# Optimization experiments

Measured on AMD Instinct MI355X. Metric: run time of the kernel, lower is better.

Reference implementation:

```python
import jax, jax.numpy as jnp
import numpy as np

N = 40000      # nodes
E = 640000     # edges (avg degree 16)
D_IN = 256     # input_size
H = 128        # hidden_size
C = 64         # num_classes
L = 2          # num_middle_layers


def spmm(val, row, col, mat):
    # sparse [N,N] @ dense [N,D]: gather neighbor rows, scale, scatter-add
    return jax.ops.segment_sum(val[:, None] * mat[col], row, num_segments=mat.shape[0])


def setup_inputs() -> dict:
    key = jax.random.key(0)
    ks = jax.random.split(key, 12)
    x = jax.random.normal(ks[0], (N, D_IN), dtype=jnp.float32)
    edge_row = jax.random.randint(ks[1], (E,), 0, N)
    edge_col = jax.random.randint(ks[2], (E,), 0, N)
    edge_val = jax.random.uniform(ks[3], (E,), dtype=jnp.float32) / 16.0  # ~normalized adjacency
    # Linear params (stored [in, out]; math equivalent to torch x @ W.T + b)
    w1 = jax.random.normal(ks[4], (D_IN, H), dtype=jnp.float32) * (1.0 / np.sqrt(D_IN))
    b1 = jax.random.normal(ks[5], (H,), dtype=jnp.float32) * 0.01
    wm = jax.random.normal(ks[6], (L, H, H), dtype=jnp.float32) * (1.0 / np.sqrt(H))
    bm = jax.random.normal(ks[7], (L, H), dtype=jnp.float32) * 0.01
    w2 = jax.random.normal(ks[8], (H, C), dtype=jnp.float32) * (1.0 / np.sqrt(H))
    b2 = jax.random.normal(ks[9], (C,), dtype=jnp.float32) * 0.01
    time_step = jnp.array(0.1, dtype=jnp.float32)
    return {"x": x, "edge_row": edge_row, "edge_col": edge_col, "edge_val": edge_val,
            "w1": w1, "b1": b1, "wm": wm, "bm": bm, "w2": w2, "b2": b2,
            "time_step": time_step}


def reference(x, edge_row, edge_col, edge_val, w1, b1, wm, bm, w2, b2, time_step):
    # dropout p=0 -> identity
    h = jax.nn.relu(spmm(edge_val, edge_row, edge_col, x @ w1 + b1))
    for i in range(L):  # residual middle layers: x <- x + relu(A @ (x W + b)) * dt
        f = jax.nn.relu(spmm(edge_val, edge_row, edge_col, h @ wm[i] + bm[i]))
        h = h + f * time_step
    return spmm(edge_val, edge_row, edge_col, h @ w2 + b2)
```

## Files before the change

kernel.cpp:

```cpp
#include <hip/hip_runtime.h>


#define DIN 256
#define HID 128
#define NCLS 64

typedef __attribute__((ext_vector_type(8))) short bf16x8;
typedef __attribute__((ext_vector_type(4))) float f32x4;

static __device__ __forceinline__ float bf2f(unsigned int u) {
    return __uint_as_float(u << 16);
}
static __device__ __forceinline__ unsigned short f2bf(float f) {
    unsigned int i = __float_as_uint(f);
    unsigned int r = (i + 0x7FFFu + ((i >> 16) & 1u)) >> 16;
    return (unsigned short)r;
}
static __device__ __forceinline__ unsigned int pack2(float a, float b) {
    return (unsigned int)f2bf(a) | ((unsigned int)f2bf(b) << 16);
}
#define VAL_DEC 1.9073486328125e-6f

__global__ void prep_kernel(const float* __restrict__ w1, const float* __restrict__ wm,
                            const float* __restrict__ w2,
                            unsigned short* __restrict__ w1t, unsigned short* __restrict__ wmt,
                            unsigned short* __restrict__ w2t, int L,
                            int* __restrict__ deg, int N) {
    int idx = blockIdx.x * blockDim.x + threadIdx.x;
    if (idx < N) deg[idx] = 0;
    int n1 = DIN * HID;
    int n2 = n1 + L * HID * HID;
    int n3 = n2 + HID * NCLS;
    if (idx < n1) {
        int n = idx / DIN, k = idx - n * DIN;
        w1t[idx] = f2bf(w1[(size_t)k * HID + n]);
    } else if (idx < n2) {
        int j = idx - n1;
        int i = j / (HID * HID), r = j - i * (HID * HID);
        int n = r / HID, k = r - n * HID;
        wmt[j] = f2bf(wm[(size_t)i * HID * HID + (size_t)k * HID + n]);
    } else if (idx < n3) {
        int j = idx - n2;
        int n = j / HID, k = j - n * HID;
        w2t[j] = f2bf(w2[(size_t)k * NCLS + n]);
    }
}


__global__ void hist_kernel(const int* __restrict__ row, int* __restrict__ deg, int E) {
    int e = blockIdx.x * blockDim.x + threadIdx.x;
    if (e < E) atomicAdd(&deg[row[e]], 1);
}

__global__ __launch_bounds__(1024) void scan_sums_kernel(
        const int* __restrict__ deg, int* __restrict__ bsums, int n) {
    __shared__ int wsum[16];
    const int lane = threadIdx.x & 63;
    const int wid  = threadIdx.x >> 6;
    int i = blockIdx.x * 1024 + threadIdx.x;
    int v = (i < n) ? deg[i] : 0;
    #pragma unroll
    for (int d = 32; d >= 1; d >>= 1) v += __shfl_xor(v, d, 64);
    if (lane == 0) wsum[wid] = v;
    __syncthreads();
    if (threadIdx.x == 0) {
        int s = 0;
        #pragma unroll
        for (int w = 0; w < 16; ++w) s += wsum[w];
        bsums[blockIdx.x] = s;
    }
}

__global__ __launch_bounds__(1024) void scan_fix_kernel(
        const int* __restrict__ deg, const int* __restrict__ bsums,
        int* __restrict__ offs, int* __restrict__ pos, int n, int nb) {
    __shared__ int wsum[16];
    __shared__ int bpref_s;
    const int lane = threadIdx.x & 63;
    const int wid  = threadIdx.x >> 6;
    const int b = blockIdx.x;
    if (wid == 0) {
        int v = (lane < nb && lane < b) ? bsums[lane] : 0;
        #pragma unroll
        for (int d = 32; d >= 1; d >>= 1) v += __shfl_xor(v, d, 64);
        if (lane == 0) bpref_s = v;
    }
    int i = b * 1024 + (int)threadIdx.x;
    int v = (i < n) ? deg[i] : 0;
    int incl = v;
    #pragma unroll
    for (int d = 1; d < 64; d <<= 1) {
        int t = __shfl_up(incl, d, 64);
        if (lane >= d) incl += t;
    }
    if (lane == 63) wsum[wid] = incl;
    __syncthreads();
    int wpref = 0;
    #pragma unroll
    for (int w = 0; w < 16; ++w)
        if (w < wid) wpref += wsum[w];
    int excl = bpref_s + wpref + incl - v;
    if (i < n) { offs[i] = excl; pos[i] = excl; }
    if (i == n) offs[n] = excl;
}

__global__ __launch_bounds__(256) void mega1_kernel(
        const float* __restrict__ x, const unsigned short* __restrict__ w1t,
        const float* __restrict__ b1, unsigned short* __restrict__ z,
        const int* __restrict__ erow, const int* __restrict__ ecol,
        const float* __restrict__ eval, int* __restrict__ pos,
        unsigned int* __restrict__ edges, int E, int gemmBlocks) {
    const int tid = threadIdx.x;
    if ((int)blockIdx.x >= gemmBlocks) {
        int nfb = gridDim.x - gemmBlocks;
        for (int e = (blockIdx.x - gemmBlocks) * 256 + tid; e < E; e += nfb * 256) {
            int r = erow[e];
            int q = min((int)(eval[e] * 524288.0f + 0.5f), 32767);
            unsigned int w = ((unsigned int)ecol[e] << 15) | (unsigned int)q;
            int p = atomicAdd(&pos[r], 1);
            edges[p] = w;
        }
        return;
    }
    __shared__ __align__(16) unsigned short Alds[64 * 40];
    __shared__ __align__(16) unsigned short Blds[128 * 40];
    const int bm   = blockIdx.x * 64;
    const int wave = tid >> 6;
    const int lane = tid & 63;
    const int m16  = lane & 15;
    const int quad = lane >> 4;
    const int ar = tid >> 2, ac = (tid & 3) * 8;

    f32x4 acc[8] = {};
    for (int k0 = 0; k0 < DIN; k0 += 32) {
        float4 a0 = *(const float4*)&x[(size_t)(bm + ar) * DIN + k0 + ac];
        float4 a1 = *(const float4*)&x[(size_t)(bm + ar) * DIN + k0 + ac + 4];
        uint4 av;
        av.x = pack2(a0.x, a0.y); av.y = pack2(a0.z, a0.w);
        av.z = pack2(a1.x, a1.y); av.w = pack2(a1.z, a1.w);
        *(uint4*)&Alds[ar * 40 + ac] = av;
        #pragma unroll
        for (int i = 0; i < 2; ++i) {
            int c  = tid + 256 * i;
            int br = c >> 2, bc = (c & 3) * 8;
            *(uint4*)&Blds[br * 40 + bc] = *(const uint4*)&w1t[(size_t)br * DIN + k0 + bc];
        }
        __syncthreads();
        bf16x8 af = *(const bf16x8*)&Alds[(wave * 16 + m16) * 40 + quad * 8];
        #pragma unroll
        for (int j = 0; j < 8; ++j) {
            bf16x8 bf = *(const bf16x8*)&Blds[(j * 16 + m16) * 40 + quad * 8];
            acc[j] = __builtin_amdgcn_mfma_f32_16x16x32_bf16(af, bf, acc[j], 0, 0, 0);
        }
        __syncthreads();
    }
    #pragma unroll
    for (int j = 0; j < 8; ++j) {
        int col = j * 16 + m16;
        float bb = b1[col];
        #pragma unroll
        for (int r = 0; r < 4; ++r) {
            int row = bm + wave * 16 + quad * 4 + r;
            z[(size_t)row * HID + col] = f2bf(acc[j][r] + bb);
        }
    }
}

template <int BN>
__global__ __launch_bounds__(256) void gemm_mfma_kernel(
        const unsigned short* __restrict__ A, const unsigned short* __restrict__ Wt,
        const float* __restrict__ bias, unsigned short* __restrict__ C, int K) {
    constexpr int NT = BN / 16;
    __shared__ __align__(16) unsigned short Alds[64 * 40];
    __shared__ __align__(16) unsigned short Blds[BN * 40];
    const int tid  = threadIdx.x;
    const int bm   = blockIdx.x * 64;
    const int wave = tid >> 6;
    const int lane = tid & 63;
    const int m16  = lane & 15;
    const int quad = lane >> 4;
    const int ar = tid >> 2, ac = (tid & 3) * 8;

    f32x4 acc[NT] = {};
    for (int k0 = 0; k0 < K; k0 += 32) {
        uint4 av = *(const uint4*)&A[(size_t)(bm + ar) * K + k0 + ac];
        *(uint4*)&Alds[ar * 40 + ac] = av;
        #pragma unroll
        for (int i = 0; i < BN / 64; ++i) {
            int c  = tid + 256 * i;
            int br = c >> 2, bc = (c & 3) * 8;
            *(uint4*)&Blds[br * 40 + bc] = *(const uint4*)&Wt[(size_t)br * K + k0 + bc];
        }
        __syncthreads();
        bf16x8 af = *(const bf16x8*)&Alds[(wave * 16 + m16) * 40 + quad * 8];
        #pragma unroll
        for (int j = 0; j < NT; ++j) {
            bf16x8 bf = *(const bf16x8*)&Blds[(j * 16 + m16) * 40 + quad * 8];
            acc[j] = __builtin_amdgcn_mfma_f32_16x16x32_bf16(af, bf, acc[j], 0, 0, 0);
        }
        __syncthreads();
    }
    #pragma unroll
    for (int j = 0; j < NT; ++j) {
        int col = j * 16 + m16;
        float bb = bias[col];
        #pragma unroll
        for (int r = 0; r < 4; ++r) {
            int row = bm + wave * 16 + quad * 4 + r;
            C[(size_t)row * BN + col] = f2bf(acc[j][r] + bb);
        }
    }
}

template <int D, int MODE>
__global__ __launch_bounds__(256) void spmm_kernel(
        const int* __restrict__ offs, const unsigned int* __restrict__ edges,
        const unsigned short* __restrict__ z,
        float* __restrict__ out, unsigned short* __restrict__ hb,
        const float* __restrict__ dt_ptr, int n) {
    int r = (int)((blockIdx.x * blockDim.x + threadIdx.x) >> 6);
    int lane = threadIdx.x & 63;
    if (r >= n) return;
    r = __builtin_amdgcn_readfirstlane(r);
    const int s = offs[r], e = offs[r + 1];
    float acc0 = 0.f, acc1 = 0.f;
    int p = s;
    if (D == 128) {
        const unsigned int* z32 = (const unsigned int*)z;
        for (; p + 8 <= e; p += 8) {
            unsigned int ev[8];
            unsigned int g[8];
            #pragma unroll
            for (int i = 0; i < 8; ++i) ev[i] = __builtin_nontemporal_load(edges + p + i);
            #pragma unroll
            for (int i = 0; i < 8; ++i)
                g[i] = z32[(size_t)(ev[i] >> 15) * 64 + lane];
            #pragma unroll
            for (int i = 0; i < 8; ++i) {
                float v = (float)(ev[i] & 0x7fffu) * VAL_DEC;
                acc0 = fmaf(v, bf2f(g[i] & 0xffffu), acc0);
                acc1 = fmaf(v, bf2f(g[i] >> 16), acc1);
            }
        }
        for (; p < e; ++p) {
            unsigned int ev = __builtin_nontemporal_load(edges + p);
            float v = (float)(ev & 0x7fffu) * VAL_DEC;
            unsigned int g = z32[(size_t)(ev >> 15) * 64 + lane];
            acc0 = fmaf(v, bf2f(g & 0xffffu), acc0);
            acc1 = fmaf(v, bf2f(g >> 16), acc1);
        }
        float2* op = (float2*)&out[(size_t)r * 128 + 2 * lane];
        float f0, f1;
        if (MODE == 0) {
            f0 = fmaxf(acc0, 0.f); f1 = fmaxf(acc1, 0.f);
            float2 o; o.x = f0; o.y = f1; *op = o;
        } else if (MODE == 1) {
            float dt = *dt_ptr;
            float2 cur = *op;
            f0 = cur.x + fmaxf(acc0, 0.f) * dt;
            f1 = cur.y + fmaxf(acc1, 0.f) * dt;
            float2 o; o.x = f0; o.y = f1; *op = o;
        } else {
            float2 o; o.x = acc0; o.y = acc1; *op = o;
            return;
        }
        __builtin_nontemporal_store(pack2(f0, f1), (unsigned int*)hb + (size_t)r * 64 + lane);
    } else {
        for (; p + 8 <= e; p += 8) {
            unsigned int ev[8];
            unsigned short g[8];
            #pragma unroll
            for (int i = 0; i < 8; ++i) ev[i] = __builtin_nontemporal_load(edges + p + i);
            #pragma unroll
            for (int i = 0; i < 8; ++i)
                g[i] = z[(size_t)(ev[i] >> 15) * 64 + lane];
            #pragma unroll
            for (int i = 0; i < 8; ++i)
                acc0 = fmaf((float)(ev[i] & 0x7fffu) * VAL_DEC, bf2f(g[i]), acc0);
        }
        for (; p < e; ++p) {
            unsigned int ev = __builtin_nontemporal_load(edges + p);
            acc0 = fmaf((float)(ev & 0x7fffu) * VAL_DEC,
                        bf2f((unsigned int)z[(size_t)(ev >> 15) * 64 + lane]), acc0);
        }
        out[(size_t)r * 64 + lane] = acc0;
    }
}

extern "C" void kernel_launch(void* const* d_in, const int* in_sizes, int n_in,
                              void* d_out, int out_size, void* d_ws, size_t ws_size,
                              hipStream_t stream) {
    const float* x    = (const float*)d_in[0];
    const int*   erow = (const int*)d_in[1];
    const int*   ecol = (const int*)d_in[2];
    const float* eval = (const float*)d_in[3];
    const float* w1   = (const float*)d_in[4];
    const float* b1   = (const float*)d_in[5];
    const float* wm   = (const float*)d_in[6];
    const float* bmp  = (const float*)d_in[7];
    const float* w2   = (const float*)d_in[8];
    const float* b2   = (const float*)d_in[9];
    const float* dt   = (const float*)d_in[10];

    const int N = in_sizes[0] / DIN;
    const int E = in_sizes[1];
    const int L = in_sizes[7] / HID;

    float* outp = (float*)d_out;

    char* ws = (char*)d_ws;
    auto carve = [&](size_t bytes) -> char* {
        char* p = ws;
        ws += (bytes + 255) & ~(size_t)255;
        return p;
    };
    int*            deg   = (int*)carve((size_t)N * 4);
    int*            bsums = (int*)carve(64 * 4);
    int*            offs  = (int*)carve((size_t)(N + 1) * 4);
    int*            pos   = (int*)carve((size_t)N * 4);
    unsigned int*   edges = (unsigned int*)carve((size_t)E * 4);
    unsigned short* z     = (unsigned short*)carve((size_t)N * HID * 2);
    float*          h     = (float*)carve((size_t)N * HID * 4);
    unsigned short* hb    = (unsigned short*)carve((size_t)N * HID * 2);
    unsigned short* w1t   = (unsigned short*)carve((size_t)HID * DIN * 2);
    unsigned short* wmt   = (unsigned short*)carve((size_t)L * HID * HID * 2);
    unsigned short* w2t   = (unsigned short*)carve((size_t)NCLS * HID * 2);

    const int ntiles = (N + 1024) / 1024;
    const int wtotal = DIN * HID + L * HID * HID + HID * NCLS;
    const int ptotal = (wtotal > N ? wtotal : N);

    prep_kernel<<<(ptotal + 255) / 256, 256, 0, stream>>>(w1, wm, w2, w1t, wmt, w2t, L, deg, N);
    hist_kernel<<<(E + 255) / 256, 256, 0, stream>>>(erow, deg, E);
    scan_sums_kernel<<<ntiles, 1024, 0, stream>>>(deg, bsums, N);
    scan_fix_kernel<<<ntiles, 1024, 0, stream>>>(deg, bsums, offs, pos, N, ntiles);

    const int gemm_blocks = N / 64;
    const int spmm_blocks = (N + 3) / 4;

    mega1_kernel<<<gemm_blocks * 2, 256, 0, stream>>>(
        x, w1t, b1, z, erow, ecol, eval, pos, edges, E, gemm_blocks);
    spmm_kernel<HID, 0><<<spmm_blocks, 256, 0, stream>>>(offs, edges, z, h, hb, nullptr, N);

    for (int i = 0; i < L; ++i) {
        gemm_mfma_kernel<HID><<<gemm_blocks, 256, 0, stream>>>(
            hb, wmt + (size_t)i * HID * HID, bmp + (size_t)i * HID, z, HID);
        spmm_kernel<HID, 1><<<spmm_blocks, 256, 0, stream>>>(offs, edges, z, h, hb, dt, N);
    }

    gemm_mfma_kernel<NCLS><<<gemm_blocks, 256, 0, stream>>>(hb, w2t, b2, z, HID);
    spmm_kernel<NCLS, 2><<<spmm_blocks, 256, 0, stream>>>(offs, edges, z, outp, nullptr, nullptr, N);
}
```

Baseline: 295.9 us.

## Replace global-atomic CSR build with two-level bucketed counting sort

Replaces the per-row global histogram and global atomic scatter with a two-level counting sort. Edges are first bucketed by row>>8 using per-block LDS histograms and a scan over bucket×block counts, then a finalize kernel sorts each bucket by its low row byte in LDS and writes offs and edges. Weight prep is folded into the histogram kernel, which drops one launch. The goal is to avoid contended global atomics and random writes, at the cost of an extra intermediate buffer pass and an extra kernel.

```diff
diff --git a/kernel.cpp b/kernel.cpp
--- a/kernel.cpp
+++ b/kernel.cpp
@@ -4,6 +4,8 @@
 #define DIN 256
 #define HID 128
 #define NCLS 64
+#define VAL_DEC 1.9073486328125e-6f
+#define SB 256
 
 typedef __attribute__((ext_vector_type(8))) short bf16x8;
 typedef __attribute__((ext_vector_type(4))) float f32x4;
@@ -13,52 +15,57 @@
 }
 static __device__ __forceinline__ unsigned short f2bf(float f) {
     unsigned int i = __float_as_uint(f);
-    unsigned int r = (i + 0x7FFFu + ((i >> 16) & 1u)) >> 16;
-    return (unsigned short)r;
+    return (unsigned short)((i + 0x7FFFu + ((i >> 16) & 1u)) >> 16);
 }
 static __device__ __forceinline__ unsigned int pack2(float a, float b) {
     return (unsigned int)f2bf(a) | ((unsigned int)f2bf(b) << 16);
 }
-#define VAL_DEC 1.9073486328125e-6f
-
-__global__ void prep_kernel(const float* __restrict__ w1, const float* __restrict__ wm,
-                            const float* __restrict__ w2,
-                            unsigned short* __restrict__ w1t, unsigned short* __restrict__ wmt,
-                            unsigned short* __restrict__ w2t, int L,
-                            int* __restrict__ deg, int N) {
-    int idx = blockIdx.x * blockDim.x + threadIdx.x;
-    if (idx < N) deg[idx] = 0;
-    int n1 = DIN * HID;
-    int n2 = n1 + L * HID * HID;
-    int n3 = n2 + HID * NCLS;
-    if (idx < n1) {
-        int n = idx / DIN, k = idx - n * DIN;
-        w1t[idx] = f2bf(w1[(size_t)k * HID + n]);
-    } else if (idx < n2) {
-        int j = idx - n1;
-        int i = j / (HID * HID), r = j - i * (HID * HID);
-        int n = r / HID, k = r - n * HID;
-        wmt[j] = f2bf(wm[(size_t)i * HID * HID + (size_t)k * HID + n]);
-    } else if (idx < n3) {
-        int j = idx - n2;
-        int n = j / HID, k = j - n * HID;
-        w2t[j] = f2bf(w2[(size_t)k * NCLS + n]);
-    }
-}
-
-
-__global__ void hist_kernel(const int* __restrict__ row, int* __restrict__ deg, int E) {
-    int e = blockIdx.x * blockDim.x + threadIdx.x;
-    if (e < E) atomicAdd(&deg[row[e]], 1);
+
+__global__ __launch_bounds__(256) void prep_hist_kernel(
+        const float* __restrict__ w1, const float* __restrict__ wm,
+        const float* __restrict__ w2, unsigned short* __restrict__ w1t,
+        unsigned short* __restrict__ wmt, unsigned short* __restrict__ w2t, int L,
+        const int* __restrict__ erow, int* __restrict__ counts_t, int E, int NB) {
+    __shared__ int cnt[256];
+    const int tid = threadIdx.x;
+    for (int k = tid; k < NB; k += 256) cnt[k] = 0;
+
+    const int n1 = DIN * HID;
+    const int n2 = n1 + L * HID * HID;
+    const int n3 = n2 + HID * NCLS;
+    for (int idx = blockIdx.x * 256 + tid; idx < n3; idx += SB * 256) {
+        if (idx < n1) {
+            int n = idx / DIN, k = idx - n * DIN;
+            w1t[idx] = f2bf(w1[(size_t)k * HID + n]);
+        } else if (idx < n2) {
+            int j = idx - n1;
+            int i = j / (HID * HID), r = j - i * (HID * HID);
+            int n = r / HID, k = r - n * HID;
+            wmt[j] = f2bf(wm[(size_t)i * HID * HID + (size_t)k * HID + n]);
+        } else {
+            int j = idx - n2;
+            int n = j / HID, k = j - n * HID;
+            w2t[j] = f2bf(w2[(size_t)k * NCLS + n]);
+        }
+    }
+    __syncthreads();
+    const int chunk = (E + SB - 1) / SB;
+    const int lo = blockIdx.x * chunk;
+    const int hi = min(lo + chunk, E);
+    for (int e = lo + tid; e < hi; e += 256)
+        atomicAdd(&cnt[erow[e] >> 8], 1);
+    __syncthreads();
+    for (int k = tid; k < NB; k += 256)
+        counts_t[k * SB + blockIdx.x] = cnt[k];
 }
 
 __global__ __launch_bounds__(1024) void scan_sums_kernel(
-        const int* __restrict__ deg, int* __restrict__ bsums, int n) {
+        const int* __restrict__ a, int* __restrict__ bsums, int n) {
     __shared__ int wsum[16];
     const int lane = threadIdx.x & 63;
     const int wid  = threadIdx.x >> 6;
     int i = blockIdx.x * 1024 + threadIdx.x;
-    int v = (i < n) ? deg[i] : 0;
+    int v = (i < n) ? a[i] : 0;
     #pragma unroll
     for (int d = 32; d >= 1; d >>= 1) v += __shfl_xor(v, d, 64);
     if (lane == 0) wsum[wid] = v;
@@ -72,8 +79,8 @@
 }
 
 __global__ __launch_bounds__(1024) void scan_fix_kernel(
-        const int* __restrict__ deg, const int* __restrict__ bsums,
-        int* __restrict__ offs, int* __restrict__ pos, int n, int nb) {
+        const int* __restrict__ a, const int* __restrict__ bsums,
+        int* __restrict__ out, int n, int nb) {
     __shared__ int wsum[16];
     __shared__ int bpref_s;
     const int lane = threadIdx.x & 63;
@@ -86,7 +93,7 @@
         if (lane == 0) bpref_s = v;
     }
     int i = b * 1024 + (int)threadIdx.x;
-    int v = (i < n) ? deg[i] : 0;
+    int v = (i < n) ? a[i] : 0;
     int incl = v;
     #pragma unroll
     for (int d = 1; d < 64; d <<= 1) {
@@ -100,25 +107,33 @@
     for (int w = 0; w < 16; ++w)
         if (w < wid) wpref += wsum[w];
     int excl = bpref_s + wpref + incl - v;
-    if (i < n) { offs[i] = excl; pos[i] = excl; }
-    if (i == n) offs[n] = excl;
-}
-
-__global__ __launch_bounds__(256) void mega1_kernel(
+    if (i < n) out[i] = excl;
+    if (i == n) out[n] = excl;
+}
+
+__global__ __launch_bounds__(256) void mega_kernel(
         const float* __restrict__ x, const unsigned short* __restrict__ w1t,
         const float* __restrict__ b1, unsigned short* __restrict__ z,
         const int* __restrict__ erow, const int* __restrict__ ecol,
-        const float* __restrict__ eval, int* __restrict__ pos,
-        unsigned int* __restrict__ edges, int E, int gemmBlocks) {
+        const float* __restrict__ eval, const int* __restrict__ starts,
+        unsigned int* __restrict__ bw, unsigned char* __restrict__ br,
+        int E, int NB, int gemmBlocks) {
     const int tid = threadIdx.x;
     if ((int)blockIdx.x >= gemmBlocks) {
-        int nfb = gridDim.x - gemmBlocks;
-        for (int e = (blockIdx.x - gemmBlocks) * 256 + tid; e < E; e += nfb * 256) {
+        __shared__ int ptr[256];
+        const int sb = blockIdx.x - gemmBlocks;
+        for (int k = tid; k < NB; k += 256) ptr[k] = starts[k * SB + sb];
+        __syncthreads();
+        const int chunk = (E + SB - 1) / SB;
+        const int lo = sb * chunk;
+        const int hi = min(lo + chunk, E);
+        for (int e = lo + tid; e < hi; e += 256) {
             int r = erow[e];
             int q = min((int)(eval[e] * 524288.0f + 0.5f), 32767);
             unsigned int w = ((unsigned int)ecol[e] << 15) | (unsigned int)q;
-            int p = atomicAdd(&pos[r], 1);
-            edges[p] = w;
+            int p = atomicAdd(&ptr[r >> 8], 1);
+            bw[p] = w;
+            br[p] = (unsigned char)(r & 255);
         }
         return;
     }
@@ -141,16 +156,16 @@
         *(uint4*)&Alds[ar * 40 + ac] = av;
         #pragma unroll
         for (int i = 0; i < 2; ++i) {
-            int c  = tid + 256 * i;
-            int br = c >> 2, bc = (c & 3) * 8;
-            *(uint4*)&Blds[br * 40 + bc] = *(const uint4*)&w1t[(size_t)br * DIN + k0 + bc];
+            int c = tid + 256 * i;
+            int brow = c >> 2, bc = (c & 3) * 8;
+            *(uint4*)&Blds[brow * 40 + bc] = *(const uint4*)&w1t[(size_t)brow * DIN + k0 + bc];
         }
         __syncthreads();
         bf16x8 af = *(const bf16x8*)&Alds[(wave * 16 + m16) * 40 + quad * 8];
         #pragma unroll
         for (int j = 0; j < 8; ++j) {
-            bf16x8 bf = *(const bf16x8*)&Blds[(j * 16 + m16) * 40 + quad * 8];
-            acc[j] = __builtin_amdgcn_mfma_f32_16x16x32_bf16(af, bf, acc[j], 0, 0, 0);
+            bf16x8 bfr = *(const bf16x8*)&Blds[(j * 16 + m16) * 40 + quad * 8];
+            acc[j] = __builtin_amdgcn_mfma_f32_16x16x32_bf16(af, bfr, acc[j], 0, 0, 0);
         }
         __syncthreads();
     }
@@ -163,6 +178,49 @@
             int row = bm + wave * 16 + quad * 4 + r;
             z[(size_t)row * HID + col] = f2bf(acc[j][r] + bb);
         }
+    }
+}
+
+__global__ __launch_bounds__(256) void finalize_kernel(
+        const int* __restrict__ starts, const unsigned int* __restrict__ bw,
+        const unsigned char* __restrict__ br, unsigned int* __restrict__ edges,
+        int* __restrict__ offs, int N, int NB) {
+    __shared__ int cnt[256];
+    __shared__ int posl[256];
+    __shared__ int ws[4];
+    const int tid = threadIdx.x;
+    const int k = blockIdx.x;
+    const int b0 = starts[k * SB];
+    const int b1 = starts[(k + 1) * SB];
+    cnt[tid] = 0;
+    __syncthreads();
+    for (int i = b0 + tid; i < b1; i += 256)
+        atomicAdd(&cnt[br[i]], 1);
+    __syncthreads();
+    const int lane = tid & 63, wid = tid >> 6;
+    int v = cnt[tid];
+    int incl = v;
+    #pragma unroll
+    for (int d = 1; d < 64; d <<= 1) {
+        int t = __shfl_up(incl, d, 64);
+        if (lane >= d) incl += t;
+    }
+    if (lane == 63) ws[wid] = incl;
+    __syncthreads();
+    int wp = 0;
+    #pragma unroll
+    for (int w = 0; w < 4; ++w)
+        if (w < wid) wp += ws[w];
+    int excl = wp + incl - v;
+    int g = (k << 8) + tid;
+    if (g <= N) offs[g] = b0 + excl;
+    posl[tid] = b0 + excl;
+    __syncthreads();
+    for (int i = b0 + tid; i < b1; i += 256) {
+        int r = br[i];
+        unsigned int w = bw[i];
+        int p = atomicAdd(&posl[r], 1);
+        edges[p] = w;
     }
 }
 
@@ -187,16 +245,16 @@
         *(uint4*)&Alds[ar * 40 + ac] = av;
         #pragma unroll
         for (int i = 0; i < BN / 64; ++i) {
-            int c  = tid + 256 * i;
-            int br = c >> 2, bc = (c & 3) * 8;
-            *(uint4*)&Blds[br * 40 + bc] = *(const uint4*)&Wt[(size_t)br * K + k0 + bc];
+            int c = tid + 256 * i;
+            int brow = c >> 2, bc = (c & 3) * 8;
+            *(uint4*)&Blds[brow * 40 + bc] = *(const uint4*)&Wt[(size_t)brow * K + k0 + bc];
         }
         __syncthreads();
         bf16x8 af = *(const bf16x8*)&Alds[(wave * 16 + m16) * 40 + quad * 8];
         #pragma unroll
         for (int j = 0; j < NT; ++j) {
-            bf16x8 bf = *(const bf16x8*)&Blds[(j * 16 + m16) * 40 + quad * 8];
-            acc[j] = __builtin_amdgcn_mfma_f32_16x16x32_bf16(af, bf, acc[j], 0, 0, 0);
+            bf16x8 bfr = *(const bf16x8*)&Blds[(j * 16 + m16) * 40 + quad * 8];
+            acc[j] = __builtin_amdgcn_mfma_f32_16x16x32_bf16(af, bfr, acc[j], 0, 0, 0);
         }
         __syncthreads();
     }
@@ -228,8 +286,7 @@
     if (D == 128) {
         const unsigned int* z32 = (const unsigned int*)z;
         for (; p + 8 <= e; p += 8) {
-            unsigned int ev[8];
-            unsigned int g[8];
+            unsigned int ev[8], g[8];
             #pragma unroll
             for (int i = 0; i < 8; ++i) ev[i] = __builtin_nontemporal_load(edges + p + i);
             #pragma unroll
@@ -305,6 +362,7 @@
     const int N = in_sizes[0] / DIN;
     const int E = in_sizes[1];
     const int L = in_sizes[7] / HID;
+    const int NB = (N + 255) >> 8;
 
     float* outp = (float*)d_out;
 
@@ -314,32 +372,33 @@
         ws += (bytes + 255) & ~(size_t)255;
         return p;
     };
-    int*            deg   = (int*)carve((size_t)N * 4);
-    int*            bsums = (int*)carve(64 * 4);
-    int*            offs  = (int*)carve((size_t)(N + 1) * 4);
-    int*            pos   = (int*)carve((size_t)N * 4);
-    unsigned int*   edges = (unsigned int*)carve((size_t)E * 4);
-    unsigned short* z     = (unsigned short*)carve((size_t)N * HID * 2);
-    float*          h     = (float*)carve((size_t)N * HID * 4);
-    unsigned short* hb    = (unsigned short*)carve((size_t)N * HID * 2);
-    unsigned short* w1t   = (unsigned short*)carve((size_t)HID * DIN * 2);
-    unsigned short* wmt   = (unsigned short*)carve((size_t)L * HID * HID * 2);
-    unsigned short* w2t   = (unsigned short*)carve((size_t)NCLS * HID * 2);
-
-    const int ntiles = (N + 1024) / 1024;
-    const int wtotal = DIN * HID + L * HID * HID + HID * NCLS;
-    const int ptotal = (wtotal > N ? wtotal : N);
-
-    prep_kernel<<<(ptotal + 255) / 256, 256, 0, stream>>>(w1, wm, w2, w1t, wmt, w2t, L, deg, N);
-    hist_kernel<<<(E + 255) / 256, 256, 0, stream>>>(erow, deg, E);
-    scan_sums_kernel<<<ntiles, 1024, 0, stream>>>(deg, bsums, N);
-    scan_fix_kernel<<<ntiles, 1024, 0, stream>>>(deg, bsums, offs, pos, N, ntiles);
-
+    int*            counts = (int*)carve((size_t)(NB * SB + 1) * 4);
+    int*            starts = (int*)carve((size_t)(NB * SB + 1) * 4);
+    int*            bsums  = (int*)carve(64 * 4);
+    int*            offs   = (int*)carve((size_t)(N + 1) * 4);
+    unsigned int*   bw     = (unsigned int*)carve((size_t)E * 4);
+    unsigned char*  brr    = (unsigned char*)carve((size_t)E);
+    unsigned int*   edges  = (unsigned int*)carve((size_t)E * 4);
+    unsigned short* z      = (unsigned short*)carve((size_t)N * HID * 2);
+    float*          h      = (float*)carve((size_t)N * HID * 4);
+    unsigned short* hb     = (unsigned short*)carve((size_t)N * HID * 2);
+    unsigned short* w1t    = (unsigned short*)carve((size_t)HID * DIN * 2);
+    unsigned short* wmt    = (unsigned short*)carve((size_t)L * HID * HID * 2);
+    unsigned short* w2t    = (unsigned short*)carve((size_t)NCLS * HID * 2);
+
+    const int nscan   = NB * SB;
+    const int ntiles  = (nscan + 1023) / 1024;
     const int gemm_blocks = N / 64;
     const int spmm_blocks = (N + 3) / 4;
 
-    mega1_kernel<<<gemm_blocks * 2, 256, 0, stream>>>(
-        x, w1t, b1, z, erow, ecol, eval, pos, edges, E, gemm_blocks);
+    prep_hist_kernel<<<SB, 256, 0, stream>>>(w1, wm, w2, w1t, wmt, w2t, L,
+                                             erow, counts, E, NB);
+    scan_sums_kernel<<<ntiles, 1024, 0, stream>>>(counts, bsums, nscan);
+    scan_fix_kernel<<<ntiles, 1024, 0, stream>>>(counts, bsums, starts, nscan, ntiles);
+    mega_kernel<<<gemm_blocks + SB, 256, 0, stream>>>(
+        x, w1t, b1, z, erow, ecol, eval, starts, bw, brr, E, NB, gemm_blocks);
+    finalize_kernel<<<NB, 256, 0, stream>>>(starts, bw, brr, edges, offs, N, NB);
+
     spmm_kernel<HID, 0><<<spmm_blocks, 256, 0, stream>>>(offs, edges, z, h, hb, nullptr, N);
 
     for (int i = 0; i < L; ++i) {
```

Measured after the change: 273.4 us. 1.08x faster.
